# Optimization experiments

Hardware: AMD Instinct MI355X
Metric: run time of the kernel (lower is better)

## Reference

```python
import jax, jax.numpy as jnp
import numpy as np
import math

B, T, E, H = 4, 2048, 1024, 16
ALPHA = 32.0


def setup_inputs() -> dict:
    key = jax.random.key(0)
    ks = jax.random.split(key, 6)
    s = 1.0 / math.sqrt(E)
    return {
        "x": jax.random.normal(ks[0], (B, T, E), dtype=jnp.float32),
        "ch_list": 0,
        "Wq": jax.random.normal(ks[1], (E, E), dtype=jnp.float32) * s,
        "bq": jnp.zeros((E,), jnp.float32),
        "Wk": jax.random.normal(ks[2], (E, E), dtype=jnp.float32) * s,
        "bk": jnp.zeros((E,), jnp.float32),
        "Wv": jax.random.normal(ks[3], (E, E), dtype=jnp.float32) * s,
        "bv": jnp.zeros((E,), jnp.float32),
        "Wp": jax.random.normal(ks[4], (E, E), dtype=jnp.float32) * s,
        "bp": jnp.zeros((E,), jnp.float32),
    }


def reference(x, ch_list, Wq, bq, Wk, bk, Wv, bv, Wp, bp):
    Bx, Tx, Ex = x.shape
    hd = Ex // H  # head dim
    # linear projections (weights stored [in, out]); split heads -> [B,H,T,hd]
    def heads(W, b):
        return (x @ W + b).reshape(Bx, Tx, H, hd).transpose(0, 2, 1, 3)
    q, k, v = heads(Wq, bq), heads(Wk, bk), heads(Wv, bv)
    scale = 1.0 / (ALPHA * math.sqrt(hd))
    qk = jnp.einsum("bhqd,bhkd->bhqk", q * scale, k)  # [B,H,T,T]
    # extra max-rescale BEFORE the causal mask (faithful to original order)
    qk = qk - jnp.max(qk, axis=-1, keepdims=True)
    causal = jnp.tril(jnp.ones((Tx, Tx), dtype=bool))  # [T,T]
    qk = jnp.where(causal[None, None], qk, -jnp.inf)
    att = jax.nn.softmax(qk * ALPHA, axis=-1)  # dropout p=0 -> identity
    y = jnp.einsum("bhqk,bhkd->bhqd", att, v)
    y = y.transpose(0, 2, 1, 3).reshape(Bx, Tx, Ex)
    return y @ Wp + bp
```

## Files before the change

kernel.cpp:

```cpp
#include <hip/hip_runtime.h>
#include <cmath>

typedef unsigned short u16;
typedef unsigned int u32;
typedef __bf16 bf16x8 __attribute__((ext_vector_type(8)));
typedef float  floatx4 __attribute__((ext_vector_type(4)));
typedef float  floatx16 __attribute__((ext_vector_type(16)));
typedef unsigned int u32x4 __attribute__((ext_vector_type(4)));

#define T_DIM 2048
#define E_DIM 1024
#define H_DIM 16
#define HD    64
#define M_DIM 8192
#define NE    8388608
#define E2    1048576
#define QSCALE 0.18033688f

__device__ __forceinline__ u16 f2bf(float f) {
    unsigned u = __builtin_bit_cast(unsigned, f);
    return (u16)((u + 0x7FFFu + ((u >> 16) & 1u)) >> 16);
}
__device__ __forceinline__ u32 pack2bf(float f0, float f1) {
    u32 a0 = __builtin_bit_cast(u32, f0) + 0x8000u;
    u32 a1 = __builtin_bit_cast(u32, f1) + 0x8000u;
    return __builtin_amdgcn_perm(a1, a0, 0x07060302u);
}

__device__ __forceinline__ void gl_lds16(const u16* g, const u16* l) {
    __builtin_amdgcn_global_load_lds(
        (const __attribute__((address_space(1))) void*)g,
        (__attribute__((address_space(3))) void*)l,
        16, 0, 0);
}

__device__ __forceinline__ bf16x8 ld_frag(const u16* p) {
    return *(const bf16x8*)p;
}

__global__ void cvt_x_kernel(const float* __restrict__ x, u16* __restrict__ xb) {
    const size_t i = (size_t)blockIdx.x * 256 + threadIdx.x;
    const float4* s = (const float4*)x + i * 2;
    const float4 a = s[0], b = s[1];
    u16 v[8] __attribute__((aligned(16)));
    v[0]=f2bf(a.x); v[1]=f2bf(a.y); v[2]=f2bf(a.z); v[3]=f2bf(a.w);
    v[4]=f2bf(b.x); v[5]=f2bf(b.y); v[6]=f2bf(b.z); v[7]=f2bf(b.w);
    *(uint4*)(xb + i * 8) = *(const uint4*)v;
}

__global__ void transpose_cvt_kernel(const float* __restrict__ w0, const float* __restrict__ w1,
                                     const float* __restrict__ w2, const float* __restrict__ w3,
                                     u16* __restrict__ out) {
    __shared__ u16 tile[64][65];
    const float* W = blockIdx.z == 0 ? w0 : blockIdx.z == 1 ? w1 : blockIdx.z == 2 ? w2 : w3;
    u16* O = out + (size_t)blockIdx.z * E2;
    const int k0 = blockIdx.y * 64, n0 = blockIdx.x * 64;
    const int r = threadIdx.x >> 2, cp = (threadIdx.x & 3) * 16;
    const float4* src = (const float4*)&W[(size_t)(k0 + r) * E_DIM + n0 + cp];
    #pragma unroll
    for (int j4 = 0; j4 < 4; ++j4) {
        const float4 f = src[j4];
        tile[r][cp + j4*4 + 0] = f2bf(f.x);
        tile[r][cp + j4*4 + 1] = f2bf(f.y);
        tile[r][cp + j4*4 + 2] = f2bf(f.z);
        tile[r][cp + j4*4 + 3] = f2bf(f.w);
    }
    __syncthreads();
    u16 vals[16] __attribute__((aligned(16)));
    #pragma unroll
    for (int j = 0; j < 16; ++j) vals[j] = tile[cp + j][r];
    u16* dst = &O[(size_t)(n0 + r) * E_DIM + k0 + cp];
    *(uint4*)dst       = *(const uint4*)vals;
    *(uint4*)(dst + 8) = *(const uint4*)(vals + 8);
}

template<int REMAP>
__global__ __launch_bounds__(256)
void gemm_bf16_kernel(const u16* __restrict__ A, const u16* __restrict__ Bt,
                      const float* __restrict__ bias0, const float* __restrict__ bias1,
                      const float* __restrict__ bias2, void* __restrict__ outp,
                      u16* __restrict__ vtp)
{
    __shared__ u16 As[128 * 32];
    __shared__ u16 Bs[128 * 32];
    const int tid = threadIdx.x;
    const int w = tid >> 6, lane = tid & 63, quad = lane >> 4, l15 = lane & 15;
    const int wm = w >> 1, wn = w & 1;
    const int r0 = blockIdx.y * 128, c0 = blockIdx.x * 128;

    floatx4 acc[4][4];
    #pragma unroll
    for (int mi = 0; mi < 4; ++mi)
        #pragma unroll
        for (int ni = 0; ni < 4; ++ni)
            acc[mi][ni] = (floatx4){0.f, 0.f, 0.f, 0.f};

    const int fsw = (quad ^ ((l15 >> 1) & 3)) * 8;

    for (int k0 = 0; k0 < E_DIM; k0 += 32) {
        __syncthreads();
        #pragma unroll
        for (int i = 0; i < 2; ++i) {
            const int L = i * 256 + tid;
            const int row = L >> 2, s = L & 3;
            const int c = s ^ ((row >> 1) & 3);
            const unsigned off = __builtin_amdgcn_readfirstlane(i * 4096 + w * 1024);
            gl_lds16(&A [(size_t)(r0 + row) * E_DIM + k0 + c * 8], (u16*)((char*)As + off));
            gl_lds16(&Bt[(size_t)(c0 + row) * E_DIM + k0 + c * 8], (u16*)((char*)Bs + off));
        }
        __syncthreads();
        bf16x8 Af[4], Bf[4];
        #pragma unroll
        for (int mi = 0; mi < 4; ++mi) Af[mi] = ld_frag(&As[(wm*64 + mi*16 + l15) * 32 + fsw]);
        #pragma unroll
        for (int ni = 0; ni < 4; ++ni) Bf[ni] = ld_frag(&Bs[(wn*64 + ni*16 + l15) * 32 + fsw]);
        #pragma unroll
        for (int mi = 0; mi < 4; ++mi)
            #pragma unroll
            for (int ni = 0; ni < 4; ++ni)
                acc[mi][ni] = __builtin_amdgcn_mfma_f32_16x16x32_bf16(Af[mi], Bf[ni], acc[mi][ni], 0, 0, 0);
    }

    #pragma unroll
    for (int ni = 0; ni < 4; ++ni) {
        const int col = c0 + wn * 64 + ni * 16 + l15;
        float bv;
        int which = 0, cc = col;
        if (REMAP == 1) {
            which = col >> 10; cc = col & 1023;
            const float* bp_ = which == 0 ? bias0 : which == 1 ? bias1 : bias2;
            bv = bp_[cc];
        } else {
            bv = bias0[col];
        }
        #pragma unroll
        for (int mi = 0; mi < 4; ++mi) {
            if (REMAP == 1 && which == 2) {
                const int h = cc >> 6, d = cc & 63;
                const int row0 = r0 + wm * 64 + mi * 16 + quad * 4;
                const int b = row0 >> 11, t0 = row0 & (T_DIM - 1);
                uint2 pk;
                pk.x = pack2bf(acc[mi][ni][0] + bv, acc[mi][ni][1] + bv);
                pk.y = pack2bf(acc[mi][ni][2] + bv, acc[mi][ni][3] + bv);
                *(uint2*)&vtp[((size_t)((b * H_DIM + h) * HD + d)) * T_DIM + t0] = pk;
            } else {
                #pragma unroll
                for (int r = 0; r < 4; ++r) {
                    const int row = r0 + wm * 64 + mi * 16 + quad * 4 + r;
                    float val = acc[mi][ni][r] + bv;
                    if (REMAP == 1) {
                        if (which == 0) val *= QSCALE;
                        const int h = cc >> 6, d = cc & 63;
                        const int b = row >> 11, t = row & (T_DIM - 1);
                        ((u16*)outp)[(size_t)which * NE +
                                     (((size_t)(b * H_DIM + h) * T_DIM + t) * HD + d)] = f2bf(val);
                    } else {
                        ((float*)outp)[(size_t)row * E_DIM + col] = val;
                    }
                }
            }
        }
    }
}

__global__ __launch_bounds__(256, 2)
void attn_kernel(const u16* __restrict__ q, const u16* __restrict__ k,
                 const u16* __restrict__ vt, u16* __restrict__ y)
{
    __shared__ u16 Ks[2][128 * 64];
    __shared__ u16 Vs[2][64 * 128];

    const int tid = threadIdx.x;
    const int w = tid >> 6, lane = tid & 63;
    const int hl = lane >> 5, l31 = lane & 31, l7 = lane & 7;
    const int bh = blockIdx.x;
    const int qt = gridDim.y - 1 - blockIdx.y;
    const int q0 = qt * 128;
    const int b = bh >> 4, h = bh & (H_DIM - 1);
    const size_t qkb = (size_t)bh * (T_DIM * HD);
    const size_t vtb = (size_t)bh * (HD * T_DIM);

    const int qrow = q0 + w * 32 + l31;
    bf16x8 Qf[4];
    #pragma unroll
    for (int kc = 0; kc < 4; ++kc)
        Qf[kc] = ld_frag(&q[qkb + (size_t)qrow * HD + kc * 16 + hl * 8]);

    float rsum = 0.f;
    floatx16 O[2];
    #pragma unroll
    for (int i = 0; i < 16; ++i) { O[0][i] = 0.f; O[1][i] = 0.f; }

    auto stage = [&](int jt, int sel) {
        const int j0 = jt * 128;
        #pragma unroll
        for (int i = 0; i < 4; ++i) {
            const int L = i * 256 + tid;
            const unsigned off = __builtin_amdgcn_readfirstlane(i * 4096 + w * 1024);
            {   const int row = L >> 3, ch = (L & 7) ^ (row & 7);
                gl_lds16(&k[qkb + (size_t)(j0 + row) * HD + ch * 8],
                         (u16*)((char*)&Ks[sel][0] + off)); }
            {   const int row = L >> 4, ch = (L & 15) ^ (row & 7);
                gl_lds16(&vt[vtb + (size_t)row * T_DIM + j0 + ch * 8],
                         (u16*)((char*)&Vs[sel][0] + off)); }
        }
    };

    stage(0, 0);
    for (int jt = 0; jt <= qt; ++jt) {
        __syncthreads();
        if (jt < qt) stage(jt + 1, (jt + 1) & 1);
        const u16* const Kb = &Ks[jt & 1][0];
        const u16* const Vb = &Vs[jt & 1][0];

        const bool diag = (jt == qt);
        const int nkg = diag ? (w + 1) : 4;

        #pragma unroll
        for (int kg = 0; kg < 4; ++kg) {
            if (kg < nkg) {
                floatx16 S;
                #pragma unroll
                for (int i = 0; i < 16; ++i) S[i] = 0.f;
                const int krow = kg * 32 + l31;
                #pragma unroll
                for (int kc = 0; kc < 4; ++kc) {
                    const int ch = (kc * 2 + hl) ^ l7;
                    S = __builtin_amdgcn_mfma_f32_32x32x16_bf16(
                            ld_frag(&Kb[krow * 64 + ch * 8]), Qf[kc], S, 0, 0, 0);
                }

                const bool bnd = diag && (kg == w);
                u32 u[8], ru[8];
                #pragma unroll
                for (int i = 0; i < 8; ++i) {
                    const int row0 = (2*i & 3) + 8 * (i >> 1) + 4 * hl;
                    float p0 = __builtin_amdgcn_exp2f(S[2*i]);
                    float p1 = __builtin_amdgcn_exp2f(S[2*i + 1]);
                    if (bnd && (row0     > l31)) p0 = 0.f;
                    if (bnd && (row0 + 1 > l31)) p1 = 0.f;
                    rsum += p0 + p1;
                    u[i] = pack2bf(p0, p1);
                }
                #pragma unroll
                for (int i = 0; i < 8; ++i) ru[i] = __shfl_xor(u[i], 32, 64);
                const u32x4 f0 = hl ? (u32x4){ru[2], ru[3], u[2], u[3]}
                                    : (u32x4){u[0], u[1], ru[0], ru[1]};
                const u32x4 f1 = hl ? (u32x4){ru[6], ru[7], u[6], u[7]}
                                    : (u32x4){u[4], u[5], ru[4], ru[5]};

                #pragma unroll
                for (int c2 = 0; c2 < 2; ++c2) {
                    const bf16x8 Pf = __builtin_bit_cast(bf16x8, c2 ? f1 : f0);
                    const int kc16 = kg * 4 + c2 * 2 + hl;
                    #pragma unroll
                    for (int dh = 0; dh < 2; ++dh) {
                        const int d = dh * 32 + l31;
                        const int ch = kc16 ^ l7;
                        O[dh] = __builtin_amdgcn_mfma_f32_32x32x16_bf16(
                                    Pf, ld_frag(&Vb[d * 128 + ch * 8]), O[dh], 0, 0, 0);
                    }
                }
            }
        }
    }

    rsum += __shfl_xor(rsum, 32, 64);
    const float linv = 1.0f / rsum;
    #pragma unroll
    for (int i = 0; i < 16; ++i) {
        const int qr = (i & 3) + 8 * (i >> 2) + 4 * hl;
        const float lq = __shfl(linv, qr, 32);
        const int t = q0 + w * 32 + qr;
        const size_t base = ((size_t)(b * T_DIM + t)) * E_DIM + h * HD;
        y[base + l31]      = f2bf(O[0][i] * lq);
        y[base + 32 + l31] = f2bf(O[1][i] * lq);
    }
}

extern "C" void kernel_launch(void* const* d_in, const int* in_sizes, int n_in,
                              void* d_out, int out_size, void* d_ws, size_t ws_size,
                              hipStream_t stream)
{
    const float* x  = (const float*)d_in[0];
    const float* Wq = (const float*)d_in[2];
    const float* bq = (const float*)d_in[3];
    const float* Wk = (const float*)d_in[4];
    const float* bk = (const float*)d_in[5];
    const float* Wv = (const float*)d_in[6];
    const float* bv = (const float*)d_in[7];
    const float* Wp = (const float*)d_in[8];
    const float* bp = (const float*)d_in[9];

    u16* xb  = (u16*)d_ws;
    u16* wt  = xb + NE;
    u16* qb  = wt + 4 * (size_t)E2;
    u16* kb  = qb + NE;
    u16* vtb = kb + NE;
    u16* yb  = vtb + NE;

    cvt_x_kernel<<<NE / (256 * 8), 256, 0, stream>>>(x, xb);
    transpose_cvt_kernel<<<dim3(16, 16, 4), 256, 0, stream>>>(Wq, Wk, Wv, Wp, wt);
    gemm_bf16_kernel<1><<<dim3(24, 64), 256, 0, stream>>>(xb, wt, bq, bk, bv, qb, vtb);
    attn_kernel<<<dim3(64, 16), 256, 0, stream>>>(qb, kb, vtb, yb);
    gemm_bf16_kernel<0><<<dim3(8, 64), 256, 0, stream>>>(yb, wt + 3 * (size_t)E2, bp, bp, bp, (float*)d_out, nullptr);
}
```

Before: 250.4 us.

## Replace GEMM with 256x256 tiled, double-buffered, ping-pong scheduled kernel

Rewrites the projection GEMM to use 256x256 output tiles with 8 waves, a 64-wide K step, and double-buffered LDS fed by asynchronous global-to-LDS loads. Fragment loads, prefetches and MFMA groups are interleaved with explicit barriers, waitcnts and setprio so that memory traffic overlaps compute. Block indices are swizzled for L2 locality. This is meant to cut global/LDS traffic per FLOP and hide load latency. The risks are 128 KB of LDS per block, lower occupancy, and only 128 blocks in the output projection, which leaves many CUs idle.

Result: slower. 263.7 us (+5.3%).

```diff
diff --git a/kernel.cpp b/kernel.cpp
--- a/kernel.cpp
+++ b/kernel.cpp
@@ -37,6 +37,9 @@
 __device__ __forceinline__ bf16x8 ld_frag(const u16* p) {
     return *(const bf16x8*)p;
 }
+
+#define S_BARRIER()  asm volatile("s_barrier" ::: "memory")
+#define WAIT_LGKM0() asm volatile("s_waitcnt lgkmcnt(0)" ::: "memory")
 
 __global__ void cvt_x_kernel(const float* __restrict__ x, u16* __restrict__ xb) {
     const size_t i = (size_t)blockIdx.x * 256 + threadIdx.x;
@@ -74,89 +77,169 @@
     *(uint4*)(dst + 8) = *(const uint4*)(vals + 8);
 }
 
+#define NT 16
+
+#define MFMA16(F0, N0, BQ)                                                          \
+    _Pragma("unroll") for (int kk = 0; kk < 2; ++kk)                                \
+    _Pragma("unroll") for (int mi = 0; mi < 4; ++mi)                                \
+    _Pragma("unroll") for (int ni = 0; ni < 2; ++ni)                                \
+        acc[(F0)+mi][(N0)+ni] = __builtin_amdgcn_mfma_f32_16x16x32_bf16(            \
+            Aq[mi][kk], BQ[ni][kk], acc[(F0)+mi][(N0)+ni], 0, 0, 0);
+
 template<int REMAP>
-__global__ __launch_bounds__(256)
-void gemm_bf16_kernel(const u16* __restrict__ A, const u16* __restrict__ Bt,
-                      const float* __restrict__ bias0, const float* __restrict__ bias1,
-                      const float* __restrict__ bias2, void* __restrict__ outp,
-                      u16* __restrict__ vtp)
+__global__ __launch_bounds__(512, 2)
+void gemm256_kernel(const u16* __restrict__ A, const u16* __restrict__ Bt,
+                    const float* __restrict__ bias0, const float* __restrict__ bias1,
+                    const float* __restrict__ bias2, void* __restrict__ outp,
+                    u16* __restrict__ vtp)
 {
-    __shared__ u16 As[128 * 32];
-    __shared__ u16 Bs[128 * 32];
+    __shared__ u16 SM[65536];
     const int tid = threadIdx.x;
     const int w = tid >> 6, lane = tid & 63, quad = lane >> 4, l15 = lane & 15;
-    const int wm = w >> 1, wn = w & 1;
-    const int r0 = blockIdx.y * 128, c0 = blockIdx.x * 128;
-
-    floatx4 acc[4][4];
-    #pragma unroll
-    for (int mi = 0; mi < 4; ++mi)
-        #pragma unroll
-        for (int ni = 0; ni < 4; ++ni)
-            acc[mi][ni] = (floatx4){0.f, 0.f, 0.f, 0.f};
-
-    const int fsw = (quad ^ ((l15 >> 1) & 3)) * 8;
-
-    for (int k0 = 0; k0 < E_DIM; k0 += 32) {
-        __syncthreads();
+    const int wm = w >> 2, wn = w & 3;
+
+    const int nbx = (REMAP == 1) ? 12 : 4;
+    const int cpx = gridDim.x >> 3;
+    const int swz = ((int)blockIdx.x & 7) * cpx + ((int)blockIdx.x >> 3);
+    const int bx = swz % nbx, by = swz / nbx;
+    const int r0 = by * 256, c0 = bx * 256;
+
+    const u16* pA[2]; const u16* pB[2]; unsigned lb[2];
+    #pragma unroll
+    for (int i = 0; i < 2; ++i) {
+        const int L = i * 512 + tid, ur = L >> 3, sl = L & 7, c = sl ^ (ur & 7);
+        const int ra = ((ur >> 6) << 7) + (ur & 63);
+        const int nb = ((ur >> 5) << 6) + (ur & 31);
+        pA[i] = A  + (size_t)(r0 + ra) * E_DIM + c * 8;
+        pB[i] = Bt + (size_t)(c0 + nb) * E_DIM + c * 8;
+        lb[i] = i * 8192u + (unsigned)w * 1024u;
+    }
+    auto stageA = [&](int kt, int u) {
         #pragma unroll
         for (int i = 0; i < 2; ++i) {
-            const int L = i * 256 + tid;
-            const int row = L >> 2, s = L & 3;
-            const int c = s ^ ((row >> 1) & 3);
-            const unsigned off = __builtin_amdgcn_readfirstlane(i * 4096 + w * 1024);
-            gl_lds16(&A [(size_t)(r0 + row) * E_DIM + k0 + c * 8], (u16*)((char*)As + off));
-            gl_lds16(&Bt[(size_t)(c0 + row) * E_DIM + k0 + c * 8], (u16*)((char*)Bs + off));
-        }
-        __syncthreads();
-        bf16x8 Af[4], Bf[4];
-        #pragma unroll
-        for (int mi = 0; mi < 4; ++mi) Af[mi] = ld_frag(&As[(wm*64 + mi*16 + l15) * 32 + fsw]);
-        #pragma unroll
-        for (int ni = 0; ni < 4; ++ni) Bf[ni] = ld_frag(&Bs[(wn*64 + ni*16 + l15) * 32 + fsw]);
-        #pragma unroll
-        for (int mi = 0; mi < 4; ++mi)
+            const unsigned off = __builtin_amdgcn_readfirstlane(
+                (unsigned)(kt & 1) * 32768u + (unsigned)u * 16384u + lb[i]);
+            gl_lds16(pA[i] + u * (64 * E_DIM) + kt * 64,
+                     (const u16*)((const char*)SM + off));
+        }
+    };
+    auto stageB = [&](int kt, int u) {
+        #pragma unroll
+        for (int i = 0; i < 2; ++i) {
+            const unsigned off = __builtin_amdgcn_readfirstlane(
+                65536u + (unsigned)(kt & 1) * 32768u + (unsigned)u * 16384u + lb[i]);
+            gl_lds16(pB[i] + u * (32 * E_DIM) + kt * 64,
+                     (const u16*)((const char*)SM + off));
+        }
+    };
+
+    const int arow = (wm * 64 + l15) * 64;
+    const int brow = (wn * 32 + l15) * 64;
+    const int sl0  = (quad ^ (l15 & 7)) * 8;
+
+    floatx4 acc[8][4];
+    #pragma unroll
+    for (int f = 0; f < 8; ++f)
+        #pragma unroll
+        for (int n = 0; n < 4; ++n) acc[f][n] = (floatx4){0.f, 0.f, 0.f, 0.f};
+
+    bf16x8 Aq[4][2], Bq0[2][2], Bq1[2][2];
+
+    stageA(0, 0); stageB(0, 0); stageA(0, 1); stageB(0, 1);
+    stageA(1, 0); stageB(1, 0); stageA(1, 1);
+    asm volatile("s_waitcnt vmcnt(6)" ::: "memory");
+    S_BARRIER();
+
+    for (int kt = 0; kt < NT; ++kt) {
+        const unsigned Ab = (unsigned)(kt & 1) * 16384u;
+        const unsigned Bb = 32768u + (unsigned)(kt & 1) * 16384u;
+
+        #pragma unroll
+        for (int mi = 0; mi < 4; ++mi) {
+            Aq[mi][0] = ld_frag(&SM[Ab + arow + mi * 1024 + sl0]);
+            Aq[mi][1] = ld_frag(&SM[Ab + arow + mi * 1024 + (sl0 ^ 32)]);
+        }
+        #pragma unroll
+        for (int ni = 0; ni < 2; ++ni) {
+            Bq0[ni][0] = ld_frag(&SM[Bb + brow + ni * 1024 + sl0]);
+            Bq0[ni][1] = ld_frag(&SM[Bb + brow + ni * 1024 + (sl0 ^ 32)]);
+        }
+        if (kt + 1 < NT) stageB(kt + 1, 1);
+        S_BARRIER(); WAIT_LGKM0();
+        __builtin_amdgcn_s_setprio(1);
+        MFMA16(0, 0, Bq0)
+        __builtin_amdgcn_s_setprio(0);
+        S_BARRIER();
+
+        #pragma unroll
+        for (int ni = 0; ni < 2; ++ni) {
+            Bq1[ni][0] = ld_frag(&SM[Bb + 8192 + brow + ni * 1024 + sl0]);
+            Bq1[ni][1] = ld_frag(&SM[Bb + 8192 + brow + ni * 1024 + (sl0 ^ 32)]);
+        }
+        if (kt + 2 < NT) stageA(kt + 2, 0);
+        S_BARRIER(); WAIT_LGKM0();
+        __builtin_amdgcn_s_setprio(1);
+        MFMA16(0, 2, Bq1)
+        __builtin_amdgcn_s_setprio(0);
+        S_BARRIER();
+
+        #pragma unroll
+        for (int mi = 0; mi < 4; ++mi) {
+            Aq[mi][0] = ld_frag(&SM[Ab + 8192 + arow + mi * 1024 + sl0]);
+            Aq[mi][1] = ld_frag(&SM[Ab + 8192 + arow + mi * 1024 + (sl0 ^ 32)]);
+        }
+        if (kt + 2 < NT) stageB(kt + 2, 0);
+        S_BARRIER(); WAIT_LGKM0();
+        __builtin_amdgcn_s_setprio(1);
+        MFMA16(4, 2, Bq1)
+        __builtin_amdgcn_s_setprio(0);
+        S_BARRIER();
+
+        if (kt + 2 < NT) stageA(kt + 2, 1);
+        S_BARRIER();
+        __builtin_amdgcn_s_setprio(1);
+        MFMA16(4, 0, Bq0)
+        __builtin_amdgcn_s_setprio(0);
+        if (kt < NT - 2)       asm volatile("s_waitcnt vmcnt(6)" ::: "memory");
+        else if (kt == NT - 2) asm volatile("s_waitcnt vmcnt(0)" ::: "memory");
+        S_BARRIER();
+    }
+
+    #pragma unroll
+    for (int n = 0; n < 4; ++n) {
+        const int col = c0 + wn * 64 + n * 16 + l15;
+        if (REMAP == 1) {
+            const int which = col >> 10, cc = col & 1023;
+            const float* bp_ = which == 0 ? bias0 : which == 1 ? bias1 : bias2;
+            const float bv = bp_[cc];
+            const int h = cc >> 6, d = cc & 63;
             #pragma unroll
-            for (int ni = 0; ni < 4; ++ni)
-                acc[mi][ni] = __builtin_amdgcn_mfma_f32_16x16x32_bf16(Af[mi], Bf[ni], acc[mi][ni], 0, 0, 0);
-    }
-
-    #pragma unroll
-    for (int ni = 0; ni < 4; ++ni) {
-        const int col = c0 + wn * 64 + ni * 16 + l15;
-        float bv;
-        int which = 0, cc = col;
-        if (REMAP == 1) {
-            which = col >> 10; cc = col & 1023;
-            const float* bp_ = which == 0 ? bias0 : which == 1 ? bias1 : bias2;
-            bv = bp_[cc];
+            for (int f = 0; f < 8; ++f) {
+                const int row0 = r0 + wm * 128 + f * 16 + quad * 4;
+                const int b = row0 >> 11, t0 = row0 & (T_DIM - 1);
+                if (which == 2) {
+                    uint2 pk;
+                    pk.x = pack2bf(acc[f][n][0] + bv, acc[f][n][1] + bv);
+                    pk.y = pack2bf(acc[f][n][2] + bv, acc[f][n][3] + bv);
+                    *(uint2*)&vtp[((size_t)((b * H_DIM + h) * HD + d)) * T_DIM + t0] = pk;
+                } else {
+                    #pragma unroll
+                    for (int r = 0; r < 4; ++r) {
+                        float val = acc[f][n][r] + bv;
+                        if (which == 0) val *= QSCALE;
+                        ((u16*)outp)[(size_t)which * NE +
+                            (((size_t)(b * H_DIM + h) * T_DIM + (t0 + r)) * HD + d)] = f2bf(val);
+                    }
+                }
+            }
         } else {
-            bv = bias0[col];
-        }
-        #pragma unroll
-        for (int mi = 0; mi < 4; ++mi) {
-            if (REMAP == 1 && which == 2) {
-                const int h = cc >> 6, d = cc & 63;
-                const int row0 = r0 + wm * 64 + mi * 16 + quad * 4;
-                const int b = row0 >> 11, t0 = row0 & (T_DIM - 1);
-                uint2 pk;
-                pk.x = pack2bf(acc[mi][ni][0] + bv, acc[mi][ni][1] + bv);
-                pk.y = pack2bf(acc[mi][ni][2] + bv, acc[mi][ni][3] + bv);
-                *(uint2*)&vtp[((size_t)((b * H_DIM + h) * HD + d)) * T_DIM + t0] = pk;
-            } else {
+            const float bv = bias0[col];
+            #pragma unroll
+            for (int f = 0; f < 8; ++f) {
                 #pragma unroll
                 for (int r = 0; r < 4; ++r) {
-                    const int row = r0 + wm * 64 + mi * 16 + quad * 4 + r;
-                    float val = acc[mi][ni][r] + bv;
-                    if (REMAP == 1) {
-                        if (which == 0) val *= QSCALE;
-                        const int h = cc >> 6, d = cc & 63;
-                        const int b = row >> 11, t = row & (T_DIM - 1);
-                        ((u16*)outp)[(size_t)which * NE +
-                                     (((size_t)(b * H_DIM + h) * T_DIM + t) * HD + d)] = f2bf(val);
-                    } else {
-                        ((float*)outp)[(size_t)row * E_DIM + col] = val;
-                    }
+                    const int row = r0 + wm * 128 + f * 16 + quad * 4 + r;
+                    ((float*)outp)[(size_t)row * E_DIM + col] = acc[f][n][r] + bv;
                 }
             }
         }
@@ -301,7 +384,7 @@
 
     cvt_x_kernel<<<NE / (256 * 8), 256, 0, stream>>>(x, xb);
     transpose_cvt_kernel<<<dim3(16, 16, 4), 256, 0, stream>>>(Wq, Wk, Wv, Wp, wt);
-    gemm_bf16_kernel<1><<<dim3(24, 64), 256, 0, stream>>>(xb, wt, bq, bk, bv, qb, vtb);
+    gemm256_kernel<1><<<384, 512, 0, stream>>>(xb, wt, bq, bk, bv, qb, vtb);
     attn_kernel<<<dim3(64, 16), 256, 0, stream>>>(qb, kb, vtb, yb);
-    gemm_bf16_kernel<0><<<dim3(8, 64), 256, 0, stream>>>(yb, wt + 3 * (size_t)E2, bp, bp, bp, (float*)d_out, nullptr);
-}
+    gemm256_kernel<0><<<128, 512, 0, stream>>>(yb, wt + 3 * (size_t)E2, bp, bp, bp, (float*)d_out, nullptr);
+}
```

## Widen GEMM K-tile to 64 and merge input conversion kernels into one launch

Applied to the files above, without the earlier changes.

The bf16 GEMM now stages a 64-wide K slice per iteration instead of 32, with a new XOR swizzle over 8 chunks and precomputed global pointers. This halves the number of barrier pairs and loop iterations per output tile, at the cost of doubled LDS per block (32 KB). The x conversion and the weight transpose/convert are fused into a single prep kernel, which removes one kernel launch.

Measured after the change: 242.4 us. -3.2%, faster.

```diff
diff --git a/kernel.cpp b/kernel.cpp
--- a/kernel.cpp
+++ b/kernel.cpp
@@ -38,23 +38,26 @@
     return *(const bf16x8*)p;
 }
 
-__global__ void cvt_x_kernel(const float* __restrict__ x, u16* __restrict__ xb) {
-    const size_t i = (size_t)blockIdx.x * 256 + threadIdx.x;
-    const float4* s = (const float4*)x + i * 2;
-    const float4 a = s[0], b = s[1];
-    u16 v[8] __attribute__((aligned(16)));
-    v[0]=f2bf(a.x); v[1]=f2bf(a.y); v[2]=f2bf(a.z); v[3]=f2bf(a.w);
-    v[4]=f2bf(b.x); v[5]=f2bf(b.y); v[6]=f2bf(b.z); v[7]=f2bf(b.w);
-    *(uint4*)(xb + i * 8) = *(const uint4*)v;
-}
-
-__global__ void transpose_cvt_kernel(const float* __restrict__ w0, const float* __restrict__ w1,
-                                     const float* __restrict__ w2, const float* __restrict__ w3,
-                                     u16* __restrict__ out) {
+__global__ void prep_kernel(const float* __restrict__ x, u16* __restrict__ xb,
+                            const float* __restrict__ w0, const float* __restrict__ w1,
+                            const float* __restrict__ w2, const float* __restrict__ w3,
+                            u16* __restrict__ out) {
     __shared__ u16 tile[64][65];
-    const float* W = blockIdx.z == 0 ? w0 : blockIdx.z == 1 ? w1 : blockIdx.z == 2 ? w2 : w3;
-    u16* O = out + (size_t)blockIdx.z * E2;
-    const int k0 = blockIdx.y * 64, n0 = blockIdx.x * 64;
+    if (blockIdx.x < 4096) {
+        const size_t i = (size_t)blockIdx.x * 256 + threadIdx.x;
+        const float4* s = (const float4*)x + i * 2;
+        const float4 a = s[0], b = s[1];
+        u16 v[8] __attribute__((aligned(16)));
+        v[0]=f2bf(a.x); v[1]=f2bf(a.y); v[2]=f2bf(a.z); v[3]=f2bf(a.w);
+        v[4]=f2bf(b.x); v[5]=f2bf(b.y); v[6]=f2bf(b.z); v[7]=f2bf(b.w);
+        *(uint4*)(xb + i * 8) = *(const uint4*)v;
+        return;
+    }
+    const int bz2 = (int)blockIdx.x - 4096;
+    const int z = bz2 >> 8, rem = bz2 & 255, byy = rem >> 4, bxx = rem & 15;
+    const float* W = z == 0 ? w0 : z == 1 ? w1 : z == 2 ? w2 : w3;
+    u16* O = out + (size_t)z * E2;
+    const int k0 = byy * 64, n0 = bxx * 64;
     const int r = threadIdx.x >> 2, cp = (threadIdx.x & 3) * 16;
     const float4* src = (const float4*)&W[(size_t)(k0 + r) * E_DIM + n0 + cp];
     #pragma unroll
@@ -81,8 +84,8 @@
                       const float* __restrict__ bias2, void* __restrict__ outp,
                       u16* __restrict__ vtp)
 {
-    __shared__ u16 As[128 * 32];
-    __shared__ u16 Bs[128 * 32];
+    __shared__ __attribute__((aligned(16))) u16 As[128 * 64];
+    __shared__ __attribute__((aligned(16))) u16 Bs[128 * 64];
     const int tid = threadIdx.x;
     const int w = tid >> 6, lane = tid & 63, quad = lane >> 4, l15 = lane & 15;
     const int wm = w >> 1, wn = w & 1;
@@ -95,30 +98,37 @@
         for (int ni = 0; ni < 4; ++ni)
             acc[mi][ni] = (floatx4){0.f, 0.f, 0.f, 0.f};
 
-    const int fsw = (quad ^ ((l15 >> 1) & 3)) * 8;
-
-    for (int k0 = 0; k0 < E_DIM; k0 += 32) {
+    const u16* pA[4]; const u16* pB[4];
+    #pragma unroll
+    for (int i = 0; i < 4; ++i) {
+        const int L = i * 256 + tid, row = L >> 3, s = L & 7, c = s ^ (row & 7);
+        pA[i] = A  + (size_t)(r0 + row) * E_DIM + c * 8;
+        pB[i] = Bt + (size_t)(c0 + row) * E_DIM + c * 8;
+    }
+
+    for (int k0 = 0; k0 < E_DIM; k0 += 64) {
         __syncthreads();
         #pragma unroll
-        for (int i = 0; i < 2; ++i) {
-            const int L = i * 256 + tid;
-            const int row = L >> 2, s = L & 3;
-            const int c = s ^ ((row >> 1) & 3);
+        for (int i = 0; i < 4; ++i) {
             const unsigned off = __builtin_amdgcn_readfirstlane(i * 4096 + w * 1024);
-            gl_lds16(&A [(size_t)(r0 + row) * E_DIM + k0 + c * 8], (u16*)((char*)As + off));
-            gl_lds16(&Bt[(size_t)(c0 + row) * E_DIM + k0 + c * 8], (u16*)((char*)Bs + off));
+            gl_lds16(pA[i] + k0, (u16*)((char*)As + off));
+            gl_lds16(pB[i] + k0, (u16*)((char*)Bs + off));
         }
         __syncthreads();
-        bf16x8 Af[4], Bf[4];
-        #pragma unroll
-        for (int mi = 0; mi < 4; ++mi) Af[mi] = ld_frag(&As[(wm*64 + mi*16 + l15) * 32 + fsw]);
-        #pragma unroll
-        for (int ni = 0; ni < 4; ++ni) Bf[ni] = ld_frag(&Bs[(wn*64 + ni*16 + l15) * 32 + fsw]);
-        #pragma unroll
-        for (int mi = 0; mi < 4; ++mi)
+        #pragma unroll
+        for (int kk = 0; kk < 2; ++kk) {
+            const int sl = ((kk * 4 + quad) ^ (l15 & 7)) * 8;
+            bf16x8 Af[4], Bf[4];
             #pragma unroll
-            for (int ni = 0; ni < 4; ++ni)
-                acc[mi][ni] = __builtin_amdgcn_mfma_f32_16x16x32_bf16(Af[mi], Bf[ni], acc[mi][ni], 0, 0, 0);
+            for (int mi = 0; mi < 4; ++mi) Af[mi] = ld_frag(&As[(wm*64 + mi*16 + l15) * 64 + sl]);
+            #pragma unroll
+            for (int ni = 0; ni < 4; ++ni) Bf[ni] = ld_frag(&Bs[(wn*64 + ni*16 + l15) * 64 + sl]);
+            #pragma unroll
+            for (int mi = 0; mi < 4; ++mi)
+                #pragma unroll
+                for (int ni = 0; ni < 4; ++ni)
+                    acc[mi][ni] = __builtin_amdgcn_mfma_f32_16x16x32_bf16(Af[mi], Bf[ni], acc[mi][ni], 0, 0, 0);
+        }
     }
 
     #pragma unroll
@@ -299,8 +309,7 @@
     u16* vtb = kb + NE;
     u16* yb  = vtb + NE;
 
-    cvt_x_kernel<<<NE / (256 * 8), 256, 0, stream>>>(x, xb);
-    transpose_cvt_kernel<<<dim3(16, 16, 4), 256, 0, stream>>>(Wq, Wk, Wv, Wp, wt);
+    prep_kernel<<<5120, 256, 0, stream>>>(x, xb, Wq, Wk, Wv, Wp, wt);
     gemm_bf16_kernel<1><<<dim3(24, 64), 256, 0, stream>>>(xb, wt, bq, bk, bv, qb, vtb);
     attn_kernel<<<dim3(64, 16), 256, 0, stream>>>(qb, kb, vtb, yb);
     gemm_bf16_kernel<0><<<dim3(8, 64), 256, 0, stream>>>(yb, wt + 3 * (size_t)E2, bp, bp, bp, (float*)d_out, nullptr);
```
